# Kernel tuning notes

Measured on AMD Instinct MI355X. Metric: run time of the kernel, lower is better.

## Reference

```python
import jax, jax.numpy as jnp
import numpy as np

N = 50000        # total nodes (2 node types x 25000)
NPER = 25000     # nodes per type
E = 600000       # edges
R = 8            # num relations
NB = 4           # num bases
IND = 256        # raw input dim per node type
HID = 128        # hidden_dim
OUT = 64         # out_dim


def setup_inputs() -> dict:
    key = jax.random.key(0)
    ks = jax.random.split(key, 24)
    s_in = 1.0 / np.sqrt(IND)
    s_h = 1.0 / np.sqrt(HID)
    d = {
        "x_paper": jax.random.normal(ks[0], (NPER, IND), jnp.float32),
        "x_author": jax.random.normal(ks[1], (NPER, IND), jnp.float32),
        "W_paper": jax.random.normal(ks[2], (IND, HID), jnp.float32) * s_in,
        "b_paper": jnp.zeros((HID,), jnp.float32),
        "W_author": jax.random.normal(ks[3], (IND, HID), jnp.float32) * s_in,
        "b_author": jnp.zeros((HID,), jnp.float32),
        "bases0": jax.random.normal(ks[4], (NB, HID, HID), jnp.float32) * s_h,
        "comp0": jax.random.normal(ks[5], (R, NB), jnp.float32) * (1.0 / np.sqrt(NB)),
        "root0": jax.random.normal(ks[6], (HID, HID), jnp.float32) * s_h,
        "bias0": jnp.zeros((HID,), jnp.float32),
        "bases1": jax.random.normal(ks[7], (NB, HID, HID), jnp.float32) * s_h,
        "comp1": jax.random.normal(ks[8], (R, NB), jnp.float32) * (1.0 / np.sqrt(NB)),
        "root1": jax.random.normal(ks[9], (HID, HID), jnp.float32) * s_h,
        "bias1": jnp.zeros((HID,), jnp.float32),
        "bases2": jax.random.normal(ks[10], (NB, HID, OUT), jnp.float32) * s_h,
        "comp2": jax.random.normal(ks[11], (R, NB), jnp.float32) * (1.0 / np.sqrt(NB)),
        "root2": jax.random.normal(ks[12], (HID, OUT), jnp.float32) * s_h,
        "bias2": jnp.zeros((OUT,), jnp.float32),
        "edge_index": jax.random.randint(ks[13], (2, E), 0, N, dtype=jnp.int64),
        "edge_type": jax.random.randint(ks[14], (E,), 0, R, dtype=jnp.int64),
    }
    return d


def rgcn_conv(x, src, dst, etype, bases, comp, root, bias):
    # weight[r] = sum_b comp[r,b] * bases[b]  -> [R, in, out]
    W = jnp.einsum('rb,bio->rio', comp, bases)
    # per-(dst node, relation) mean aggregation (PyG RGCNConv default aggr='mean')
    seg = dst * R + etype                                   # [E]
    cnt = jax.ops.segment_sum(jnp.ones((E,), x.dtype), seg, num_segments=N * R)
    norm = 1.0 / jnp.maximum(cnt, 1.0)                      # [N*R]
    msg = x[src] * norm[seg][:, None]                       # [E, in]
    agg = jax.ops.segment_sum(msg, seg, num_segments=N * R) # [N*R, in]
    agg = agg.reshape(N, R, x.shape[1])                     # [N, R, in]
    return jnp.einsum('nri,rio->no', agg, W) + x @ root + bias


def reference(x_paper, x_author, W_paper, b_paper, W_author, b_author,
              bases0, comp0, root0, bias0,
              bases1, comp1, root1, bias1,
              bases2, comp2, root2, bias2,
              edge_index, edge_type):
    # Lazy linear projections + ReLU (dropout is identity in eval mode)
    hp = jax.nn.relu(x_paper @ W_paper + b_paper)
    ha = jax.nn.relu(x_author @ W_author + b_author)
    x = jnp.concatenate([hp, ha], axis=0)                   # [N, HID]

    src, dst = edge_index[0], edge_index[1]
    x_latents = [x]

    # conv 0 (i == 0: replace)
    h = jax.nn.relu(rgcn_conv(x, src, dst, edge_type, bases0, comp0, root0, bias0))
    x_latents.append(x)
    x = h

    # conv 1 (i > 0: residual add)
    h = jax.nn.relu(rgcn_conv(x, src, dst, edge_type, bases1, comp1, root1, bias1))
    x_latents.append(x)
    x = x + h

    # final conv
    out = rgcn_conv(x, src, dst, edge_type, bases2, comp2, root2, bias2)
    return (out, x_latents)
```

## Files before the change

kernel.cpp:

```cpp
#include <hip/hip_runtime.h>
#include <stdint.h>

#define NPER  25000
#define NNODE 50000
#define NEDGE 600000
#define NREL  8
#define NBASE 4
#define INDIM 256
#define HIDD  128
#define OUTD  64
#define NSEG  (NNODE * NREL)

typedef unsigned short u16;
typedef unsigned int   u32;
typedef __attribute__((ext_vector_type(8))) __bf16          bf16x8;
typedef __attribute__((ext_vector_type(8))) unsigned short  ushort8;
typedef __attribute__((ext_vector_type(4))) float           f32x4;

__device__ __forceinline__ u16 f2b(float f) {
    union { __bf16 h; u16 u; } v; v.h = (__bf16)f; return v.u;
}
__device__ __forceinline__ bf16x8 as_bf(ushort8 u) {
    union { ushort8 a; bf16x8 b; } v; v.a = u; return v.b;
}
__device__ __forceinline__ bf16x8 cvt8(const float* p) {
    f32x4 f0 = *(const f32x4*)p;
    f32x4 f1 = *(const f32x4*)(p + 4);
    ushort8 u;
#pragma unroll
    for (int i = 0; i < 4; i++) { u[i] = f2b(f0[i]); u[i + 4] = f2b(f1[i]); }
    return as_bf(u);
}
__device__ __forceinline__ float blo(u32 v) {
    union { u32 i; float f; } u; u.i = v << 16; return u.f;
}
__device__ __forceinline__ float bhi(u32 v) {
    union { u32 i; float f; } u; u.i = v & 0xffff0000u; return u.f;
}

__device__ __forceinline__ void bsw_proj_elem(const float* __restrict__ W, u16* __restrict__ out, int idx) {
    int j    = idx & 7;
    int lane = (idx >> 3) & 63;
    int rest = idx >> 9;
    int nt   = rest & 7;
    int ks   = rest >> 3;
    int col  = nt * 16 + (lane & 15);
    int k    = ks * 32 + ((lane >> 4) << 3) + j;
    out[idx] = f2b(W[(size_t)k * 128 + col]);
}
__device__ __forceinline__ void bsw_conv_elem(const float* __restrict__ bases, const float* __restrict__ root,
                                              int ncol, u16* __restrict__ out, int idx) {
    int nt_cnt = ncol >> 4;
    int j    = idx & 7;
    int lane = (idx >> 3) & 63;
    int rest = idx >> 9;
    int nt   = rest % nt_cnt;
    int ks   = rest / nt_cnt;
    int col  = nt * 16 + (lane & 15);
    int k    = ks * 32 + ((lane >> 4) << 3) + j;
    float v = (k < 512) ? bases[(size_t)k * ncol + col] : root[(size_t)(k - 512) * ncol + col];
    out[idx] = f2b(v);
}
__global__ void build_bsw_all(const float* __restrict__ Wp, const float* __restrict__ Wa,
                              const float* __restrict__ bases0, const float* __restrict__ root0,
                              const float* __restrict__ bases1, const float* __restrict__ root1,
                              const float* __restrict__ bases2, const float* __restrict__ root2,
                              u16* __restrict__ Bswp, u16* __restrict__ Bswa,
                              u16* __restrict__ Bswc0, u16* __restrict__ Bswc1, u16* __restrict__ Bswc2) {
    int b = blockIdx.x, t = threadIdx.x;
    if (b < 128)       bsw_proj_elem(Wp, Bswp, b * 256 + t);
    else if (b < 256)  bsw_proj_elem(Wa, Bswa, (b - 128) * 256 + t);
    else if (b < 576)  bsw_conv_elem(bases0, root0, HIDD, Bswc0, (b - 256) * 256 + t);
    else if (b < 896)  bsw_conv_elem(bases1, root1, HIDD, Bswc1, (b - 576) * 256 + t);
    else               bsw_conv_elem(bases2, root2, OUTD, Bswc2, (b - 896) * 256 + t);
}

__global__ void hist_kernel(const int* __restrict__ ei, const int* __restrict__ et,
                            int* __restrict__ cnt) {
    int e = blockIdx.x * blockDim.x + threadIdx.x;
    if (e >= NEDGE) return;
    int dst = ei[NEDGE + e];
    int r   = et[e];
    atomicAdd(&cnt[dst * NREL + r], 1);
}

#define SCAN_CHUNK 1024
__global__ void scan1_kernel(int* __restrict__ data, int n, int* __restrict__ bsum) {
    __shared__ int sh[256];
    int t = threadIdx.x;
    int base = blockIdx.x * SCAN_CHUNK + t * 4;
    int v[4];
#pragma unroll
    for (int i = 0; i < 4; i++) v[i] = (base + i < n) ? data[base + i] : 0;
    int tot = v[0] + v[1] + v[2] + v[3];
    sh[t] = tot; __syncthreads();
    for (int off = 1; off < 256; off <<= 1) {
        int x = (t >= off) ? sh[t - off] : 0;
        __syncthreads();
        sh[t] += x;
        __syncthreads();
    }
    int excl = sh[t] - tot;
    if (t == 255) bsum[blockIdx.x] = sh[255];
    int run = excl;
#pragma unroll
    for (int i = 0; i < 4; i++) {
        if (base + i < n) data[base + i] = run;
        run += v[i];
    }
}

__global__ void scan2_kernel(int* __restrict__ bsum, int nb) {
    __shared__ int sh[512];
    int t = threadIdx.x;
    int v = (t < nb) ? bsum[t] : 0;
    sh[t] = v; __syncthreads();
    for (int off = 1; off < 512; off <<= 1) {
        int x = (t >= off) ? sh[t - off] : 0;
        __syncthreads();
        sh[t] += x;
        __syncthreads();
    }
    if (t < nb) bsum[t] = sh[t] - v;
}

__global__ void scan3_kernel(int* __restrict__ data, int n, const int* __restrict__ bsum,
                             int* __restrict__ fill) {
    int add = bsum[blockIdx.x];
    int base = blockIdx.x * SCAN_CHUNK + threadIdx.x * 4;
#pragma unroll
    for (int i = 0; i < 4; i++) {
        int idx = base + i;
        if (idx < n) {
            int v = data[idx] + add;
            data[idx] = v;
            if (idx < NSEG) fill[idx] = v;
        }
    }
}

__global__ void scatter_kernel(const int* __restrict__ ei, const int* __restrict__ et,
                               int* __restrict__ fill, int* __restrict__ epk) {
    int e = blockIdx.x * blockDim.x + threadIdx.x;
    if (e >= NEDGE) return;
    int src = ei[e];
    int dst = ei[NEDGE + e];
    int r   = et[e];
    int pos = atomicAdd(&fill[dst * NREL + r], 1);
    epk[pos] = src | (r << 16);
}

__global__ __launch_bounds__(256) void agg_kernel(
    const u16* __restrict__ xbf, const float* __restrict__ comp,
    const int* __restrict__ rowptr, const int* __restrict__ epk,
    u16* __restrict__ Abuf) {
    __shared__ float wtab[4][40];
    int tid  = threadIdx.x;
    int wv   = __builtin_amdgcn_readfirstlane(tid >> 6);
    int lane = tid & 63;
    int node = blockIdx.x * 4 + wv;
    int rbase = node * NREL;
    if (lane < 36) {
        float wval = 0.f;
        if (lane < 32) {
            int r  = lane >> 2;
            int c0 = rowptr[rbase + r], c1 = rowptr[rbase + r + 1];
            int cnt = c1 - c0;
            float nrm = (cnt > 0) ? 1.f / (float)cnt : 0.f;
            wval = comp[lane] * nrm;
        }
        wtab[wv][lane] = wval;
    }
    __syncthreads();
    const float* wt = &wtab[wv][0];
    int p = __builtin_amdgcn_readfirstlane(rowptr[rbase]);
    int e = __builtin_amdgcn_readfirstlane(rowptr[rbase + 8]);
    int co = lane * 2;
    const int INV = 8 << 16;
    float a0[4] = {0.f, 0.f, 0.f, 0.f};
    float a1[4] = {0.f, 0.f, 0.f, 0.f};
    int k0[4]; u32 v0[4];
#pragma unroll
    for (int i = 0; i < 4; i++) k0[i] = (p + i < e) ? epk[p + i] : INV;
#pragma unroll
    for (int i = 0; i < 4; i++) v0[i] = *(const u32*)(xbf + ((size_t)(k0[i] & 0xffff) << 7) + co);
    for (int pc = p; pc < e; pc += 4) {
        int pn = pc + 4;
        int k1[4]; u32 v1[4];
#pragma unroll
        for (int i = 0; i < 4; i++) k1[i] = (pn + i < e) ? epk[pn + i] : INV;
#pragma unroll
        for (int i = 0; i < 4; i++) v1[i] = *(const u32*)(xbf + ((size_t)(k1[i] & 0xffff) << 7) + co);
#pragma unroll
        for (int i = 0; i < 4; i++) {
            f32x4 w = *(const f32x4*)(wt + ((k0[i] >> 16) << 2));
            float xl = blo(v0[i]), xh = bhi(v0[i]);
#pragma unroll
            for (int b = 0; b < 4; b++) { a0[b] += w[b] * xl; a1[b] += w[b] * xh; }
        }
#pragma unroll
        for (int i = 0; i < 4; i++) { k0[i] = k1[i]; v0[i] = v1[i]; }
    }
    size_t ob = (size_t)node * 512 + co;
#pragma unroll
    for (int b = 0; b < 4; b++) {
        u32 pk = (u32)f2b(a0[b]) | ((u32)f2b(a1[b]) << 16);
        *(u32*)(Abuf + ob + b * 128) = pk;
    }
}

template<int KMAIN, bool HASX, int NW, int MW, int NT, bool RELU, bool RES, bool AF32>
__device__ __forceinline__ void gemm_core(
    int blk, const void* __restrict__ Av, const u16* __restrict__ xq,
    const u16* __restrict__ Bsw, const float* __restrict__ bias, int M,
    float* __restrict__ out1, float* __restrict__ out2, u16* __restrict__ outb,
    const float* __restrict__ resid, int ldo) {
    constexpr int KSM = KMAIN / 32;
    constexpr int KST = KSM + (HASX ? 4 : 0);
    int tid  = threadIdx.x;
    int wave = tid >> 6, lane = tid & 63;
    int l15  = lane & 15, quad = lane >> 4;
    int rowbase = blk * (NW * MW * 16) + wave * (MW * 16);
    int rA[MW];
#pragma unroll
    for (int m = 0; m < MW; m++) {
        rA[m] = rowbase + m * 16 + l15;
        if (rA[m] > M - 1) rA[m] = M - 1;
    }
    const u16* bp = Bsw + lane * 8;
    f32x4 acc[MW][NT];
#pragma unroll
    for (int m = 0; m < MW; m++)
#pragma unroll
        for (int i = 0; i < NT; i++) acc[m][i] = (f32x4){0.f, 0.f, 0.f, 0.f};
#pragma unroll
    for (int ks = 0; ks < KST; ks++) {
        bf16x8 a[MW];
#pragma unroll
        for (int m = 0; m < MW; m++) {
            if (ks < KSM) {
                if (AF32) a[m] = cvt8((const float*)Av + (size_t)rA[m] * KMAIN + ks * 32 + quad * 8);
                else      a[m] = as_bf(*(const ushort8*)((const u16*)Av + (size_t)rA[m] * KMAIN + ks * 32 + quad * 8));
            } else {
                a[m] = as_bf(*(const ushort8*)(xq + (size_t)rA[m] * 128 + (ks - KSM) * 32 + quad * 8));
            }
        }
#pragma unroll
        for (int nt = 0; nt < NT; nt++) {
            bf16x8 b = as_bf(*(const ushort8*)(bp + ((size_t)(ks * NT + nt) << 9)));
#pragma unroll
            for (int m = 0; m < MW; m++)
                acc[m][nt] = __builtin_amdgcn_mfma_f32_16x16x32_bf16(a[m], b, acc[m][nt], 0, 0, 0);
        }
    }
#pragma unroll
    for (int m = 0; m < MW; m++) {
        int orow0 = rowbase + m * 16 + quad * 4;
#pragma unroll
        for (int r = 0; r < 4; r++) {
            int orow = orow0 + r;
            if (orow < M) {
#pragma unroll
                for (int nt = 0; nt < NT; nt++) {
                    int col = nt * 16 + l15;
                    float v = acc[m][nt][r] + bias[col];
                    if (RELU) v = v > 0.f ? v : 0.f;
                    if (RES)  v += resid[(size_t)orow * ldo + col];
                    size_t oi = (size_t)orow * ldo + col;
                    if (out1) out1[oi] = v;
                    if (out2) out2[oi] = v;
                    if (outb) outb[oi] = f2b(v);
                }
            }
        }
    }
}

template<int KMAIN, bool HASX, int NW, int MW, int NT, bool RELU, bool RES, bool AF32>
__global__ __launch_bounds__(NW * 64, 2) void gemm_kernel(
    const void* __restrict__ Av, const u16* __restrict__ xq,
    const u16* __restrict__ Bsw, const float* __restrict__ bias, int M,
    float* __restrict__ out1, float* __restrict__ out2, u16* __restrict__ outb,
    const float* __restrict__ resid, int ldo) {
    gemm_core<KMAIN, HASX, NW, MW, NT, RELU, RES, AF32>(
        blockIdx.x, Av, xq, Bsw, bias, M, out1, out2, outb, resid, ldo);
}

__global__ __launch_bounds__(256, 2) void proj2_kernel(
    const float* __restrict__ xp, const float* __restrict__ xa,
    const u16* __restrict__ Bswp, const u16* __restrict__ Bswa,
    const float* __restrict__ bp, const float* __restrict__ ba,
    float* __restrict__ lat0, float* __restrict__ lat1, u16* __restrict__ xbf0) {
    int y = blockIdx.y;
    const float* A    = y ? xa : xp;
    const u16*   B    = y ? Bswa : Bswp;
    const float* bias = y ? ba : bp;
    size_t off = (size_t)y * NPER * HIDD;
    gemm_core<256, false, 4, 1, 8, true, false, true>(
        blockIdx.x, A, nullptr, B, bias, NPER, lat0 + off, lat1 + off, xbf0 + off, nullptr, HIDD);
}

extern "C" void kernel_launch(void* const* d_in, const int* in_sizes, int n_in,
                              void* d_out, int out_size, void* d_ws, size_t ws_size,
                              hipStream_t stream) {
    const float* x_paper  = (const float*)d_in[0];
    const float* x_author = (const float*)d_in[1];
    const float* W_paper  = (const float*)d_in[2];
    const float* b_paper  = (const float*)d_in[3];
    const float* W_author = (const float*)d_in[4];
    const float* b_author = (const float*)d_in[5];
    const float* bases0   = (const float*)d_in[6];
    const float* comp0    = (const float*)d_in[7];
    const float* root0    = (const float*)d_in[8];
    const float* bias0    = (const float*)d_in[9];
    const float* bases1   = (const float*)d_in[10];
    const float* comp1    = (const float*)d_in[11];
    const float* root1    = (const float*)d_in[12];
    const float* bias1    = (const float*)d_in[13];
    const float* bases2   = (const float*)d_in[14];
    const float* comp2    = (const float*)d_in[15];
    const float* root2    = (const float*)d_in[16];
    const float* bias2    = (const float*)d_in[17];
    const int* ei         = (const int*)d_in[18];
    const int* et         = (const int*)d_in[19];

    float* ob   = (float*)d_out;
    float* outF = ob;
    float* lat0 = ob + 3200000;
    float* lat1 = ob + 9600000;
    float* lat2 = ob + 16000000;

    char* w = (char*)d_ws;
    u16*   Abuf   = (u16*)(w + 0);
    u16*   xbf0   = (u16*)(w + 51200000);
    u16*   xbf1   = (u16*)(w + 64000000);
    u16*   Bswc0  = (u16*)(w + 76800000);
    u16*   Bswc1  = (u16*)(w + 76963840);
    u16*   Bswc2  = (u16*)(w + 77127680);
    u16*   Bswp   = (u16*)(w + 77209600);
    u16*   Bswa   = (u16*)(w + 77275136);
    int*   rowptr = (int*)(w + 77340672);
    int*   fill   = (int*)(w + 78940736);
    int*   epk    = (int*)(w + 80540736);
    int*   bsum   = (int*)(w + 82940736);

    build_bsw_all<<<1056, 256, 0, stream>>>(W_paper, W_author, bases0, root0,
                                            bases1, root1, bases2, root2,
                                            Bswp, Bswa, Bswc0, Bswc1, Bswc2);

    proj2_kernel<<<dim3((NPER + 63) / 64, 2), 256, 0, stream>>>(
        x_paper, x_author, Bswp, Bswa, b_paper, b_author, lat0, lat1, xbf0);

    hipMemsetAsync(rowptr, 0, (NSEG + 1) * sizeof(int), stream);
    hist_kernel<<<(NEDGE + 255) / 256, 256, 0, stream>>>(ei, et, rowptr);
    int nchunk = (NSEG + 1 + SCAN_CHUNK - 1) / SCAN_CHUNK;
    scan1_kernel<<<nchunk, 256, 0, stream>>>(rowptr, NSEG + 1, bsum);
    scan2_kernel<<<1, 512, 0, stream>>>(bsum, nchunk);
    scan3_kernel<<<nchunk, 256, 0, stream>>>(rowptr, NSEG + 1, bsum, fill);
    scatter_kernel<<<(NEDGE + 255) / 256, 256, 0, stream>>>(ei, et, fill, epk);

    agg_kernel<<<NNODE / 4, 256, 0, stream>>>(xbf0, comp0, rowptr, epk, Abuf);
    gemm_kernel<512, true, 2, 2, 8, true, false, false><<<(NNODE + 63) / 64, 128, 0, stream>>>(
        Abuf, xbf0, Bswc0, bias0, NNODE, lat2, nullptr, xbf1, nullptr, HIDD);

    agg_kernel<<<NNODE / 4, 256, 0, stream>>>(xbf1, comp1, rowptr, epk, Abuf);
    gemm_kernel<512, true, 2, 2, 8, true, true, false><<<(NNODE + 63) / 64, 128, 0, stream>>>(
        Abuf, xbf1, Bswc1, bias1, NNODE, nullptr, nullptr, xbf0, lat2, HIDD);

    agg_kernel<<<NNODE / 4, 256, 0, stream>>>(xbf0, comp2, rowptr, epk, Abuf);
    gemm_kernel<512, true, 2, 2, 4, false, false, false><<<(NNODE + 63) / 64, 128, 0, stream>>>(
        Abuf, xbf0, Bswc2, bias2, NNODE, outF, nullptr, nullptr, nullptr, OUTD);
}
```

Baseline: 462.0 us.

## Fuse per-node relation aggregation with basis GEMM in shared memory

Replaces the separate aggregation kernel and GEMM kernel per conv layer with one fused kernel. Each block aggregates 64 nodes into a swizzled bf16 LDS tile and then runs MFMA against the basis/root weights directly. This removes the global Abuf round trip of 51 MB write plus read per layer and cuts the launch count. Per-relation weights now come from cross-lane readlane instead of an LDS table. The cost is 64KB of LDS per block, which limits occupancy, and serialized per-wave node loops with no overlap between the gather and MFMA phases.

```diff
diff --git a/kernel.cpp b/kernel.cpp
--- a/kernel.cpp
+++ b/kernel.cpp
@@ -150,62 +150,114 @@
     epk[pos] = src | (r << 16);
 }
 
-__global__ __launch_bounds__(256) void agg_kernel(
+template<int NT, bool RELU, bool RES>
+__global__ __launch_bounds__(256, 2) void fused_conv(
     const u16* __restrict__ xbf, const float* __restrict__ comp,
     const int* __restrict__ rowptr, const int* __restrict__ epk,
-    u16* __restrict__ Abuf) {
-    __shared__ float wtab[4][40];
+    const u16* __restrict__ Bsw, const float* __restrict__ bias,
+    float* __restrict__ out1, u16* __restrict__ outb,
+    const float* __restrict__ resid, int ldo) {
+    __shared__ u16 As[64 * 512];
     int tid  = threadIdx.x;
     int wv   = __builtin_amdgcn_readfirstlane(tid >> 6);
     int lane = tid & 63;
-    int node = blockIdx.x * 4 + wv;
-    int rbase = node * NREL;
-    if (lane < 36) {
-        float wval = 0.f;
-        if (lane < 32) {
-            int r  = lane >> 2;
-            int c0 = rowptr[rbase + r], c1 = rowptr[rbase + r + 1];
-            int cnt = c1 - c0;
-            float nrm = (cnt > 0) ? 1.f / (float)cnt : 0.f;
-            wval = comp[lane] * nrm;
-        }
-        wtab[wv][lane] = wval;
+    int co   = lane * 2;
+    float compv = (lane < 32) ? comp[lane] : 0.f;
+    const int INV = 8 << 16;
+
+    for (int i = 0; i < 16; i++) {
+        int node = blockIdx.x * 64 + wv * 16 + i;
+        int lr   = wv * 16 + i;
+        float a0[4] = {0.f, 0.f, 0.f, 0.f};
+        float a1[4] = {0.f, 0.f, 0.f, 0.f};
+        int p = 0, e = 0;
+        float wl = 0.f;
+        if (node < NNODE) {
+            int rbase = node * NREL;
+            if (lane < 32) {
+                int r   = lane >> 2;
+                int c0  = rowptr[rbase + r], c1 = rowptr[rbase + r + 1];
+                int cnt = c1 - c0;
+                float nrm = (cnt > 0) ? 1.f / (float)cnt : 0.f;
+                wl = compv * nrm;
+            }
+            p = __builtin_amdgcn_readfirstlane(rowptr[rbase]);
+            e = __builtin_amdgcn_readfirstlane(rowptr[rbase + 8]);
+        }
+        int k0[4]; u32 v0[4];
+#pragma unroll
+        for (int j = 0; j < 4; j++) k0[j] = (p + j < e) ? epk[p + j] : INV;
+#pragma unroll
+        for (int j = 0; j < 4; j++) v0[j] = *(const u32*)(xbf + ((size_t)(k0[j] & 0xffff) << 7) + co);
+        for (int pc = p; pc < e; pc += 4) {
+            int pn = pc + 4;
+            int k1[4]; u32 v1[4];
+#pragma unroll
+            for (int j = 0; j < 4; j++) k1[j] = (pn + j < e) ? epk[pn + j] : INV;
+#pragma unroll
+            for (int j = 0; j < 4; j++) v1[j] = *(const u32*)(xbf + ((size_t)(k1[j] & 0xffff) << 7) + co);
+#pragma unroll
+            for (int j = 0; j < 4; j++) {
+                int ri = __builtin_amdgcn_readfirstlane((k0[j] >> 16) << 2);
+                float w0 = __uint_as_float(__builtin_amdgcn_readlane(__float_as_uint(wl), ri));
+                float w1 = __uint_as_float(__builtin_amdgcn_readlane(__float_as_uint(wl), ri + 1));
+                float w2 = __uint_as_float(__builtin_amdgcn_readlane(__float_as_uint(wl), ri + 2));
+                float w3 = __uint_as_float(__builtin_amdgcn_readlane(__float_as_uint(wl), ri + 3));
+                float xl = blo(v0[j]), xh = bhi(v0[j]);
+                a0[0] += w0 * xl; a1[0] += w0 * xh;
+                a0[1] += w1 * xl; a1[1] += w1 * xh;
+                a0[2] += w2 * xl; a1[2] += w2 * xh;
+                a0[3] += w3 * xl; a1[3] += w3 * xh;
+            }
+#pragma unroll
+            for (int j = 0; j < 4; j++) { k0[j] = k1[j]; v0[j] = v1[j]; }
+        }
+        u32 swz = (u32)(lr & 7) << 4;
+        char* rowp = (char*)As + lr * 1024;
+#pragma unroll
+        for (int b = 0; b < 4; b++) {
+            u32 pk = (u32)f2b(a0[b]) | ((u32)f2b(a1[b]) << 16);
+            *(u32*)(rowp + (((u32)(b * 256 + lane * 4)) ^ swz)) = pk;
+        }
     }
     __syncthreads();
-    const float* wt = &wtab[wv][0];
-    int p = __builtin_amdgcn_readfirstlane(rowptr[rbase]);
-    int e = __builtin_amdgcn_readfirstlane(rowptr[rbase + 8]);
-    int co = lane * 2;
-    const int INV = 8 << 16;
-    float a0[4] = {0.f, 0.f, 0.f, 0.f};
-    float a1[4] = {0.f, 0.f, 0.f, 0.f};
-    int k0[4]; u32 v0[4];
-#pragma unroll
-    for (int i = 0; i < 4; i++) k0[i] = (p + i < e) ? epk[p + i] : INV;
-#pragma unroll
-    for (int i = 0; i < 4; i++) v0[i] = *(const u32*)(xbf + ((size_t)(k0[i] & 0xffff) << 7) + co);
-    for (int pc = p; pc < e; pc += 4) {
-        int pn = pc + 4;
-        int k1[4]; u32 v1[4];
-#pragma unroll
-        for (int i = 0; i < 4; i++) k1[i] = (pn + i < e) ? epk[pn + i] : INV;
-#pragma unroll
-        for (int i = 0; i < 4; i++) v1[i] = *(const u32*)(xbf + ((size_t)(k1[i] & 0xffff) << 7) + co);
-#pragma unroll
-        for (int i = 0; i < 4; i++) {
-            f32x4 w = *(const f32x4*)(wt + ((k0[i] >> 16) << 2));
-            float xl = blo(v0[i]), xh = bhi(v0[i]);
-#pragma unroll
-            for (int b = 0; b < 4; b++) { a0[b] += w[b] * xl; a1[b] += w[b] * xh; }
-        }
-#pragma unroll
-        for (int i = 0; i < 4; i++) { k0[i] = k1[i]; v0[i] = v1[i]; }
-    }
-    size_t ob = (size_t)node * 512 + co;
-#pragma unroll
-    for (int b = 0; b < 4; b++) {
-        u32 pk = (u32)f2b(a0[b]) | ((u32)f2b(a1[b]) << 16);
-        *(u32*)(Abuf + ob + b * 128) = pk;
+
+    int l15 = lane & 15, quad = lane >> 4;
+    int rowbase = blockIdx.x * 64 + wv * 16;
+    int xrow = rowbase + l15; if (xrow > NNODE - 1) xrow = NNODE - 1;
+    const u16*  bp   = Bsw + lane * 8;
+    const char* arow = (const char*)As + (wv * 16 + l15) * 1024;
+    u32 swz2 = (u32)(l15 & 7) << 4;
+    f32x4 acc[NT];
+#pragma unroll
+    for (int nt = 0; nt < NT; nt++) acc[nt] = (f32x4){0.f, 0.f, 0.f, 0.f};
+#pragma unroll
+    for (int ks = 0; ks < 20; ks++) {
+        bf16x8 a;
+        if (ks < 16) a = *(const bf16x8*)(arow + (((u32)(ks * 64 + quad * 16)) ^ swz2));
+        else         a = as_bf(*(const ushort8*)(xbf + (size_t)xrow * 128 + (ks - 16) * 32 + quad * 8));
+#pragma unroll
+        for (int nt = 0; nt < NT; nt++) {
+            bf16x8 b = as_bf(*(const ushort8*)(bp + ((size_t)(ks * NT + nt) << 9)));
+            acc[nt] = __builtin_amdgcn_mfma_f32_16x16x32_bf16(a, b, acc[nt], 0, 0, 0);
+        }
+    }
+    int orow0 = rowbase + quad * 4;
+#pragma unroll
+    for (int r = 0; r < 4; r++) {
+        int orow = orow0 + r;
+        if (orow < NNODE) {
+#pragma unroll
+            for (int nt = 0; nt < NT; nt++) {
+                int col = nt * 16 + l15;
+                float v = acc[nt][r] + bias[col];
+                if (RELU) v = v > 0.f ? v : 0.f;
+                if (RES)  v += resid[(size_t)orow * ldo + col];
+                size_t oi = (size_t)orow * ldo + col;
+                if (out1) out1[oi] = v;
+                if (outb) outb[oi] = f2b(v);
+            }
+        }
     }
 }
 
@@ -274,16 +326,6 @@
             }
         }
     }
-}
-
-template<int KMAIN, bool HASX, int NW, int MW, int NT, bool RELU, bool RES, bool AF32>
-__global__ __launch_bounds__(NW * 64, 2) void gemm_kernel(
-    const void* __restrict__ Av, const u16* __restrict__ xq,
-    const u16* __restrict__ Bsw, const float* __restrict__ bias, int M,
-    float* __restrict__ out1, float* __restrict__ out2, u16* __restrict__ outb,
-    const float* __restrict__ resid, int ldo) {
-    gemm_core<KMAIN, HASX, NW, MW, NT, RELU, RES, AF32>(
-        blockIdx.x, Av, xq, Bsw, bias, M, out1, out2, outb, resid, ldo);
 }
 
 __global__ __launch_bounds__(256, 2) void proj2_kernel(
@@ -331,7 +373,6 @@
     float* lat2 = ob + 16000000;
 
     char* w = (char*)d_ws;
-    u16*   Abuf   = (u16*)(w + 0);
     u16*   xbf0   = (u16*)(w + 51200000);
     u16*   xbf1   = (u16*)(w + 64000000);
     u16*   Bswc0  = (u16*)(w + 76800000);
@@ -359,15 +400,14 @@
     scan3_kernel<<<nchunk, 256, 0, stream>>>(rowptr, NSEG + 1, bsum, fill);
     scatter_kernel<<<(NEDGE + 255) / 256, 256, 0, stream>>>(ei, et, fill, epk);
 
-    agg_kernel<<<NNODE / 4, 256, 0, stream>>>(xbf0, comp0, rowptr, epk, Abuf);
-    gemm_kernel<512, true, 2, 2, 8, true, false, false><<<(NNODE + 63) / 64, 128, 0, stream>>>(
-        Abuf, xbf0, Bswc0, bias0, NNODE, lat2, nullptr, xbf1, nullptr, HIDD);
-
-    agg_kernel<<<NNODE / 4, 256, 0, stream>>>(xbf1, comp1, rowptr, epk, Abuf);
-    gemm_kernel<512, true, 2, 2, 8, true, true, false><<<(NNODE + 63) / 64, 128, 0, stream>>>(
-        Abuf, xbf1, Bswc1, bias1, NNODE, nullptr, nullptr, xbf0, lat2, HIDD);
-
-    agg_kernel<<<NNODE / 4, 256, 0, stream>>>(xbf0, comp2, rowptr, epk, Abuf);
-    gemm_kernel<512, true, 2, 2, 4, false, false, false><<<(NNODE + 63) / 64, 128, 0, stream>>>(
-        Abuf, xbf0, Bswc2, bias2, NNODE, outF, nullptr, nullptr, nullptr, OUTD);
-}
+    int ngrid = (NNODE + 63) / 64;
+
+    fused_conv<8, true, false><<<ngrid, 256, 0, stream>>>(
+        xbf0, comp0, rowptr, epk, Bswc0, bias0, lat2, xbf1, nullptr, HIDD);
+
+    fused_conv<8, true, true><<<ngrid, 256, 0, stream>>>(
+        xbf1, comp1, rowptr, epk, Bswc1, bias1, nullptr, xbf0, lat2, HIDD);
+
+    fused_conv<4, false, false><<<ngrid, 256, 0, stream>>>(
+        xbf0, comp2, rowptr, epk, Bswc2, bias2, outF, nullptr, nullptr, OUTD);
+}
```

Result: slower. 577.7 us (+25.0%).
